# Kernel optimization log

Measured on AMD Instinct MI355X. Metric: run time of the kernel, lower is better.

Reference implementation:

```python
import jax, jax.numpy as jnp
import numpy as np

EMBED_DIM = 512
NUM_HEADS = 8
HEAD_DIM = EMBED_DIM // NUM_HEADS


def setup_inputs() -> dict:
    key = jax.random.key(0)
    k1, k2, kw, kb, kow, kob = jax.random.split(key, 6)
    B, L, C = 2, 2048, EMBED_DIM
    s = 1.0 / np.sqrt(C)
    return {
        "x1": jax.random.normal(k1, (B, L, C), dtype=jnp.float32),
        "x2": jax.random.normal(k2, (B, L, C), dtype=jnp.float32),
        # nn.Linear(embed_dim, 3*embed_dim): weight [3C, C], bias [3C]
        "qkv_w": jax.random.uniform(kw, (3 * C, C), jnp.float32, -s, s),
        "qkv_b": jax.random.uniform(kb, (3 * C,), jnp.float32, -s, s),
        # nn.Linear(embed_dim, embed_dim): weight [C, C], bias [C]
        "out_w": jax.random.uniform(kow, (C, C), jnp.float32, -s, s),
        "out_b": jax.random.uniform(kob, (C,), jnp.float32, -s, s),
    }


def _qkv(x, qkv_w, qkv_b):
    B, L, C = x.shape
    H, D = NUM_HEADS, C // NUM_HEADS
    # Linear: x @ W^T + b, then view(B, L, H, 3, D) and split along the '3' axis
    qkv = (jnp.einsum("blc,fc->blf", x, qkv_w) + qkv_b).reshape(B, L, H, 3, D)
    qkv = jnp.transpose(qkv, (3, 0, 2, 1, 4))  # [3, B, H, L, D]
    return qkv[0], qkv[1], qkv[2]


def _attend(q, k, v):
    # q,k,v: [B, H, L, D]; scale by 1/sqrt(D)
    scale = 1.0 / np.sqrt(q.shape[-1]).astype(np.float32)
    scores = jnp.einsum("bhqd,bhkd->bhqk", q, k) * scale  # [B,H,L,L]
    attn = jax.nn.softmax(scores, axis=-1)
    out = jnp.einsum("bhqk,bhkd->bhqd", attn, v)
    B, H, L, D = out.shape
    return jnp.transpose(out, (0, 2, 1, 3)).reshape(B, L, H * D)


def reference(x1, x2, qkv_w, qkv_b, out_w, out_b):
    q1, k1, v1 = _qkv(x1, qkv_w, qkv_b)
    q2, k2, v2 = _qkv(x2, qkv_w, qkv_b)
    out1 = _attend(q1, k2, v2)  # q from x1, k/v from x2
    out2 = _attend(q2, k1, v1)  # q from x2, k/v from x1
    out1 = jnp.einsum("blc,fc->blf", out1, out_w) + out_b
    out2 = jnp.einsum("blc,fc->blf", out2, out_w) + out_b
    return (out1, out2)
```

## Files before the change

### kernel.cpp

```cpp
#include <hip/hip_runtime.h>
#include <stdint.h>

typedef unsigned short u16;
typedef unsigned int u32;
typedef short bf16x8 __attribute__((ext_vector_type(8)));
typedef float f32x4 __attribute__((ext_vector_type(4)));

#define K_DIM 512

__device__ __forceinline__ u16 f2bf(float f) {
  union { float f; u32 u; } v; v.f = f;
  return (u16)((v.u + 0x8000u) >> 16);
}
__device__ __forceinline__ u32 pk2(float lo, float hi) {
  union { float f; u32 u; } a, b; a.f = lo; b.f = hi;
  return __builtin_amdgcn_perm(b.u + 0x8000u, a.u + 0x8000u, 0x07060302u);
}

__global__ void cvt_kernel(const float* __restrict__ x1, const float* __restrict__ x2,
                           const float* __restrict__ qkvw, const float* __restrict__ outw,
                           u16* __restrict__ xb, u16* __restrict__ wqkv, u16* __restrict__ wout) {
  int tid = blockIdx.x * 256 + threadIdx.x;
  const float4* src; u16* dst; int idx = tid;
  if (idx < 524288)        { src = (const float4*)x1;   dst = xb; }
  else if (idx < 1048576)  { src = (const float4*)x2;   dst = xb + 2097152; idx -= 524288; }
  else if (idx < 1245184)  { src = (const float4*)qkvw; dst = wqkv;         idx -= 1048576; }
  else                     { src = (const float4*)outw; dst = wout;         idx -= 1245184; }
  float4 v = src[idx];
  *(uint2*)&dst[idx * 4] = make_uint2(pk2(v.x, v.y), pk2(v.z, v.w));
}

#define LDA 40

__global__ __launch_bounds__(256, 3) void qkv_gemm(
    const u16* __restrict__ A, const u16* __restrict__ W, const float* __restrict__ bias,
    u16* __restrict__ qb, u16* __restrict__ kb, u16* __restrict__ vtb) {
  __shared__ __align__(16) u16 As[2][128 * LDA];
  __shared__ __align__(16) u16 Bs[2][128 * LDA];
  const int t = threadIdx.x;
  const int m0 = blockIdx.x * 128, n0 = blockIdx.y * 128;
  const int lane = t & 63, l16 = lane & 15, quad = lane >> 4;
  const int w = t >> 6;
  const int wm = (w >> 1) * 64, wn = (w & 1) * 64;
  const int sr = t >> 2, sc = (t & 3) * 8;

  const u16* Ap = A + (size_t)(m0 + sr) * K_DIM + sc;
  const u16* Wp = W + (size_t)(n0 + sr) * K_DIM + sc;

  f32x4 acc[4][4];
#pragma unroll
  for (int i = 0; i < 4; ++i)
#pragma unroll
    for (int j = 0; j < 4; ++j) acc[i][j] = (f32x4){0.f, 0.f, 0.f, 0.f};

  uint4 ra0 = *(const uint4*)(Ap);
  uint4 ra1 = *(const uint4*)(Ap + 64 * K_DIM);
  uint4 rb0 = *(const uint4*)(Wp);
  uint4 rb1 = *(const uint4*)(Wp + 64 * K_DIM);
  *(uint4*)&As[0][sr * LDA + sc] = ra0;
  *(uint4*)&As[0][(sr + 64) * LDA + sc] = ra1;
  *(uint4*)&Bs[0][sr * LDA + sc] = rb0;
  *(uint4*)&Bs[0][(sr + 64) * LDA + sc] = rb1;
  ra0 = *(const uint4*)(Ap + 32);
  ra1 = *(const uint4*)(Ap + 64 * K_DIM + 32);
  rb0 = *(const uint4*)(Wp + 32);
  rb1 = *(const uint4*)(Wp + 64 * K_DIM + 32);
  __syncthreads();

  for (int kt = 0; kt < 16; ++kt) {
    const int cur = kt & 1, nxt = cur ^ 1;
    if (kt < 15) {
      *(uint4*)&As[nxt][sr * LDA + sc] = ra0;
      *(uint4*)&As[nxt][(sr + 64) * LDA + sc] = ra1;
      *(uint4*)&Bs[nxt][sr * LDA + sc] = rb0;
      *(uint4*)&Bs[nxt][(sr + 64) * LDA + sc] = rb1;
    }
    if (kt < 14) {
      int ko = (kt + 2) * 32;
      ra0 = *(const uint4*)(Ap + ko);
      ra1 = *(const uint4*)(Ap + 64 * K_DIM + ko);
      rb0 = *(const uint4*)(Wp + ko);
      rb1 = *(const uint4*)(Wp + 64 * K_DIM + ko);
    }
    bf16x8 af[4], bfr[4];
#pragma unroll
    for (int mi = 0; mi < 4; ++mi)
      af[mi] = *(const bf16x8*)&As[cur][(wm + mi * 16 + l16) * LDA + quad * 8];
#pragma unroll
    for (int ni = 0; ni < 4; ++ni)
      bfr[ni] = *(const bf16x8*)&Bs[cur][(wn + ni * 16 + l16) * LDA + quad * 8];
#pragma unroll
    for (int mi = 0; mi < 4; ++mi)
#pragma unroll
      for (int ni = 0; ni < 4; ++ni)
        acc[mi][ni] = __builtin_amdgcn_mfma_f32_16x16x32_bf16(bfr[ni], af[mi], acc[mi][ni], 0, 0, 0);
    __syncthreads();
  }

  const int fbase = n0 + wn;
  const int h = fbase / 192;
  const int s = (fbase - h * 192) >> 6;
  float4 bv[4];
#pragma unroll
  for (int ni = 0; ni < 4; ++ni)
    bv[ni] = *(const float4*)&bias[fbase + ni * 16 + quad * 4];
  const int bh = m0 >> 11;
  const int lbase = (m0 & 2047) + wm;

  if (s == 2) {
    u16* dst = vtb + (size_t)((bh * 8 + h) * 64) * 2048;
#pragma unroll
    for (int mi = 0; mi < 4; ++mi) {
      int l = lbase + mi * 16 + l16;
#pragma unroll
      for (int ni = 0; ni < 4; ++ni)
#pragma unroll
        for (int r = 0; r < 4; ++r)
          dst[(ni * 16 + quad * 4 + r) * 2048 + l] = f2bf(acc[mi][ni][r] + bv[ni][r]);
    }
  } else {
    u16* dst = (s == 0 ? qb : kb) + (size_t)((bh * 8 + h) * 2048) * 64;
    const float sc2 = (s == 0) ? 0.18033688011112042f : 1.0f;
#pragma unroll
    for (int mi = 0; mi < 4; ++mi) {
      int l = lbase + mi * 16 + l16;
#pragma unroll
      for (int ni = 0; ni < 4; ++ni) {
        float v0 = (acc[mi][ni][0] + bv[ni][0]) * sc2;
        float v1 = (acc[mi][ni][1] + bv[ni][1]) * sc2;
        float v2 = (acc[mi][ni][2] + bv[ni][2]) * sc2;
        float v3 = (acc[mi][ni][3] + bv[ni][3]) * sc2;
        *(uint2*)&dst[(size_t)l * 64 + ni * 16 + quad * 4] = make_uint2(pk2(v0, v1), pk2(v2, v3));
      }
    }
  }
}

#define LQ 72
#define LP 72

__global__ __launch_bounds__(512, 4) void attn_kernel(
    const u16* __restrict__ qb, const u16* __restrict__ kb, const u16* __restrict__ vtb,
    u16* __restrict__ attnb) {
  __shared__ __align__(16) u16 Ks[64 * LQ];
  __shared__ __align__(16) u16 VTs[64 * LQ];
  __shared__ __align__(16) u16 Ps[128 * LP];

  const int t = threadIdx.x;
  const int w = t >> 6, lane = t & 63, l16 = lane & 15, quad = lane >> 4;
  const int bid = blockIdx.x;
  const int qt = bid & 15;
  const int comb = bid >> 4;
  const int h = comb & 7, bb = (comb >> 3) & 1, pair = comb >> 4;
  const int in_q = pair, in_kv = pair ^ 1;

  const u16* Qg = qb + (size_t)((in_q * 2 + bb) * 8 + h) * 2048 * 64;
  const u16* Kg = kb + (size_t)((in_kv * 2 + bb) * 8 + h) * 2048 * 64;
  const u16* Vg = vtb + (size_t)((in_kv * 2 + bb) * 8 + h) * 64 * 2048;

#pragma unroll
  for (int u = 0; u < 2; ++u) {
    int idx = u * 512 + t;
    int row = idx >> 3, seg = (idx & 7) * 8;
    *(uint4*)&Ps[row * LP + seg] = *(const uint4*)(Qg + (qt * 128 + row) * 64 + seg);
  }
  const int srow = t >> 3, sseg = (t & 7) * 8;
  uint4 rk = *(const uint4*)(Kg + srow * 64 + sseg);
  uint4 rv = *(const uint4*)(Vg + srow * 2048 + sseg);
  __syncthreads();

  bf16x8 qf[2];
#pragma unroll
  for (int ks = 0; ks < 2; ++ks)
    qf[ks] = *(const bf16x8*)&Ps[(w * 16 + l16) * LP + ks * 32 + quad * 8];

  f32x4 oacc[4];
  float rs = 0.f;
#pragma unroll
  for (int ni = 0; ni < 4; ++ni) oacc[ni] = (f32x4){0.f, 0.f, 0.f, 0.f};

  u16* Pw = &Ps[w * 16 * LP];

  for (int kt = 0; kt < 32; ++kt) {
    *(uint4*)&Ks[srow * LQ + sseg] = rk;
    *(uint4*)&VTs[srow * LQ + sseg] = rv;
    __syncthreads();
    if (kt < 31) {
      int ko = (kt + 1) * 64;
      rk = *(const uint4*)(Kg + (ko + srow) * 64 + sseg);
      rv = *(const uint4*)(Vg + srow * 2048 + ko + sseg);
    }

    f32x4 sacc[4];
#pragma unroll
    for (int ni = 0; ni < 4; ++ni) sacc[ni] = (f32x4){0.f, 0.f, 0.f, 0.f};
#pragma unroll
    for (int ks = 0; ks < 2; ++ks) {
      bf16x8 kfr[4];
#pragma unroll
      for (int ni = 0; ni < 4; ++ni)
        kfr[ni] = *(const bf16x8*)&Ks[(ni * 16 + l16) * LQ + ks * 32 + quad * 8];
#pragma unroll
      for (int ni = 0; ni < 4; ++ni)
        sacc[ni] = __builtin_amdgcn_mfma_f32_16x16x32_bf16(kfr[ni], qf[ks], sacc[ni], 0, 0, 0);
    }

#pragma unroll
    for (int ni = 0; ni < 4; ++ni) {
      float p0 = __builtin_amdgcn_exp2f(sacc[ni][0]);
      float p1 = __builtin_amdgcn_exp2f(sacc[ni][1]);
      float p2 = __builtin_amdgcn_exp2f(sacc[ni][2]);
      float p3 = __builtin_amdgcn_exp2f(sacc[ni][3]);
      rs += (p0 + p1) + (p2 + p3);
      *(uint2*)&Pw[l16 * LP + ni * 16 + quad * 4] = make_uint2(pk2(p0, p1), pk2(p2, p3));
    }

#pragma unroll
    for (int ks = 0; ks < 2; ++ks) {
      bf16x8 vf[4];
#pragma unroll
      for (int ni = 0; ni < 4; ++ni)
        vf[ni] = *(const bf16x8*)&VTs[(ni * 16 + l16) * LQ + ks * 32 + quad * 8];
      bf16x8 pf = *(const bf16x8*)&Pw[l16 * LP + ks * 32 + quad * 8];
#pragma unroll
      for (int ni = 0; ni < 4; ++ni)
        oacc[ni] = __builtin_amdgcn_mfma_f32_16x16x32_bf16(vf[ni], pf, oacc[ni], 0, 0, 0);
    }
    __syncthreads();
  }

  float s = rs;
  s += __shfl_xor(s, 16);
  s += __shfl_xor(s, 32);
  const float inv = 1.0f / s;
  const int row = in_q * 4096 + bb * 2048 + qt * 128 + w * 16 + l16;
#pragma unroll
  for (int ni = 0; ni < 4; ++ni) {
    float v0 = oacc[ni][0] * inv;
    float v1 = oacc[ni][1] * inv;
    float v2 = oacc[ni][2] * inv;
    float v3 = oacc[ni][3] * inv;
    *(uint2*)&attnb[(size_t)row * 512 + h * 64 + ni * 16 + quad * 4] =
        make_uint2(pk2(v0, v1), pk2(v2, v3));
  }
}

__global__ __launch_bounds__(256, 2) void out_gemm(
    const u16* __restrict__ A, const u16* __restrict__ W, const float* __restrict__ bias,
    float* __restrict__ out) {
  __shared__ __align__(16) u16 As[2][64 * LDA];
  __shared__ __align__(16) u16 Bs[2][128 * LDA];
  const int t = threadIdx.x;
  const int m0 = blockIdx.x * 64, n0 = blockIdx.y * 128;
  const int lane = t & 63, l16 = lane & 15, quad = lane >> 4;
  const int w = t >> 6;
  const int wm = (w & 1) * 32, wn = (w >> 1) * 64;
  const int ar = t >> 2, ac = (t & 3) * 8;
  const int sr = t >> 2, sc = (t & 3) * 8;

  const u16* Ap = A + (size_t)(m0 + ar) * K_DIM + ac;
  const u16* Wp = W + (size_t)(n0 + sr) * K_DIM + sc;

  f32x4 acc[2][4];
#pragma unroll
  for (int i = 0; i < 2; ++i)
#pragma unroll
    for (int j = 0; j < 4; ++j) acc[i][j] = (f32x4){0.f, 0.f, 0.f, 0.f};

  uint4 ra = *(const uint4*)Ap;
  uint4 rb0 = *(const uint4*)(Wp);
  uint4 rb1 = *(const uint4*)(Wp + 64 * K_DIM);
  *(uint4*)&As[0][ar * LDA + ac] = ra;
  *(uint4*)&Bs[0][sr * LDA + sc] = rb0;
  *(uint4*)&Bs[0][(sr + 64) * LDA + sc] = rb1;
  ra = *(const uint4*)(Ap + 32);
  rb0 = *(const uint4*)(Wp + 32);
  rb1 = *(const uint4*)(Wp + 64 * K_DIM + 32);
  __syncthreads();

  for (int kt = 0; kt < 16; ++kt) {
    const int cur = kt & 1, nxt = cur ^ 1;
    if (kt < 15) {
      *(uint4*)&As[nxt][ar * LDA + ac] = ra;
      *(uint4*)&Bs[nxt][sr * LDA + sc] = rb0;
      *(uint4*)&Bs[nxt][(sr + 64) * LDA + sc] = rb1;
    }
    if (kt < 14) {
      int ko = (kt + 2) * 32;
      ra = *(const uint4*)(Ap + ko);
      rb0 = *(const uint4*)(Wp + ko);
      rb1 = *(const uint4*)(Wp + 64 * K_DIM + ko);
    }
    bf16x8 af[2], bfr[4];
#pragma unroll
    for (int mi = 0; mi < 2; ++mi)
      af[mi] = *(const bf16x8*)&As[cur][(wm + mi * 16 + l16) * LDA + quad * 8];
#pragma unroll
    for (int ni = 0; ni < 4; ++ni)
      bfr[ni] = *(const bf16x8*)&Bs[cur][(wn + ni * 16 + l16) * LDA + quad * 8];
#pragma unroll
    for (int mi = 0; mi < 2; ++mi)
#pragma unroll
      for (int ni = 0; ni < 4; ++ni)
        acc[mi][ni] = __builtin_amdgcn_mfma_f32_16x16x32_bf16(af[mi], bfr[ni], acc[mi][ni], 0, 0, 0);
    __syncthreads();
  }

#pragma unroll
  for (int ni = 0; ni < 4; ++ni) {
    int f = n0 + wn + ni * 16 + l16;
    float bv = bias[f];
#pragma unroll
    for (int mi = 0; mi < 2; ++mi)
#pragma unroll
      for (int r = 0; r < 4; ++r) {
        int m = m0 + wm + mi * 16 + quad * 4 + r;
        out[(size_t)m * 512 + f] = acc[mi][ni][r] + bv;
      }
  }
}

extern "C" void kernel_launch(void* const* d_in, const int* in_sizes, int n_in,
                              void* d_out, int out_size, void* d_ws, size_t ws_size,
                              hipStream_t stream) {
  const float* x1   = (const float*)d_in[0];
  const float* x2   = (const float*)d_in[1];
  const float* qkvw = (const float*)d_in[2];
  const float* qkvb = (const float*)d_in[3];
  const float* outw = (const float*)d_in[4];
  const float* outb = (const float*)d_in[5];
  float* out = (float*)d_out;
  char* ws = (char*)d_ws;

  u16* xb    = (u16*)(ws + 0);
  u16* wqkv  = (u16*)(ws + 8388608);
  u16* wout  = (u16*)(ws + 9961472);
  u16* qb    = (u16*)(ws + 10485760);
  u16* kb    = (u16*)(ws + 18874368);
  u16* vtb   = (u16*)(ws + 27262976);
  u16* attnb = (u16*)(ws + 0);

  cvt_kernel<<<5120, 256, 0, stream>>>(x1, x2, qkvw, outw, xb, wqkv, wout);

  dim3 g1(64, 12);
  qkv_gemm<<<g1, 256, 0, stream>>>(xb, wqkv, qkvb, qb, kb, vtb);

  attn_kernel<<<512, 512, 0, stream>>>(qb, kb, vtb, attnb);

  dim3 g3(128, 4);
  out_gemm<<<g3, 256, 0, stream>>>(attnb, wout, outb, out);
}
```

Baseline: 164.4 us.

## Switch attention to 32x32 MFMA with 4 waves each owning 32 query rows

The attention kernel now runs 256 threads (4 waves) per block instead of 512. Each wave handles 32 query rows and uses 32x32x16 bf16 MFMA for both QK^T and PV, replacing the 16x16x32 tiles. This halves the number of LDS fragment reads of K and V per MFMA and raises the work per wave. The block index mapping also changes so that consecutive blocks cover different heads and batches rather than different query tiles. The trade-offs are fewer waves per block for hiding latency and more accumulator registers per thread.

Result: faster. 156.3 us (-4.9%).

```diff
diff --git a/kernel.cpp b/kernel.cpp
--- a/kernel.cpp
+++ b/kernel.cpp
@@ -5,6 +5,7 @@
 typedef unsigned int u32;
 typedef short bf16x8 __attribute__((ext_vector_type(8)));
 typedef float f32x4 __attribute__((ext_vector_type(4)));
+typedef float f32x16 __attribute__((ext_vector_type(16)));
 
 #define K_DIM 512
 
@@ -139,7 +140,7 @@
 #define LQ 72
 #define LP 72
 
-__global__ __launch_bounds__(512, 4) void attn_kernel(
+__global__ __launch_bounds__(256, 2) void attn_kernel(
     const u16* __restrict__ qb, const u16* __restrict__ kb, const u16* __restrict__ vtb,
     u16* __restrict__ attnb) {
   __shared__ __align__(16) u16 Ks[64 * LQ];
@@ -147,10 +148,10 @@
   __shared__ __align__(16) u16 Ps[128 * LP];
 
   const int t = threadIdx.x;
-  const int w = t >> 6, lane = t & 63, l16 = lane & 15, quad = lane >> 4;
+  const int w = t >> 6, lane = t & 63, l32 = lane & 31, h2 = lane >> 5;
   const int bid = blockIdx.x;
-  const int qt = bid & 15;
-  const int comb = bid >> 4;
+  const int comb = bid & 31;
+  const int qt = bid >> 5;
   const int h = comb & 7, bb = (comb >> 3) & 1, pair = comb >> 4;
   const int in_q = pair, in_kv = pair ^ 1;
 
@@ -159,90 +160,96 @@
   const u16* Vg = vtb + (size_t)((in_kv * 2 + bb) * 8 + h) * 64 * 2048;
 
 #pragma unroll
-  for (int u = 0; u < 2; ++u) {
-    int idx = u * 512 + t;
+  for (int u = 0; u < 4; ++u) {
+    int idx = u * 256 + t;
     int row = idx >> 3, seg = (idx & 7) * 8;
     *(uint4*)&Ps[row * LP + seg] = *(const uint4*)(Qg + (qt * 128 + row) * 64 + seg);
   }
   const int srow = t >> 3, sseg = (t & 7) * 8;
-  uint4 rk = *(const uint4*)(Kg + srow * 64 + sseg);
-  uint4 rv = *(const uint4*)(Vg + srow * 2048 + sseg);
+  uint4 rk0 = *(const uint4*)(Kg + srow * 64 + sseg);
+  uint4 rk1 = *(const uint4*)(Kg + (srow + 32) * 64 + sseg);
+  uint4 rv0 = *(const uint4*)(Vg + srow * 2048 + sseg);
+  uint4 rv1 = *(const uint4*)(Vg + (srow + 32) * 2048 + sseg);
   __syncthreads();
 
-  bf16x8 qf[2];
-#pragma unroll
-  for (int ks = 0; ks < 2; ++ks)
-    qf[ks] = *(const bf16x8*)&Ps[(w * 16 + l16) * LP + ks * 32 + quad * 8];
-
-  f32x4 oacc[4];
+  bf16x8 qf[4];
+#pragma unroll
+  for (int ks = 0; ks < 4; ++ks)
+    qf[ks] = *(const bf16x8*)&Ps[(w * 32 + l32) * LP + ks * 16 + h2 * 8];
+
+  f32x16 oacc[2];
+#pragma unroll
+  for (int mi = 0; mi < 2; ++mi)
+#pragma unroll
+    for (int r = 0; r < 16; ++r) oacc[mi][r] = 0.f;
   float rs = 0.f;
-#pragma unroll
-  for (int ni = 0; ni < 4; ++ni) oacc[ni] = (f32x4){0.f, 0.f, 0.f, 0.f};
-
-  u16* Pw = &Ps[w * 16 * LP];
+
+  u16* Pw = &Ps[w * 32 * LP];
 
   for (int kt = 0; kt < 32; ++kt) {
-    *(uint4*)&Ks[srow * LQ + sseg] = rk;
-    *(uint4*)&VTs[srow * LQ + sseg] = rv;
+    *(uint4*)&Ks[srow * LQ + sseg] = rk0;
+    *(uint4*)&Ks[(srow + 32) * LQ + sseg] = rk1;
+    *(uint4*)&VTs[srow * LQ + sseg] = rv0;
+    *(uint4*)&VTs[(srow + 32) * LQ + sseg] = rv1;
     __syncthreads();
     if (kt < 31) {
       int ko = (kt + 1) * 64;
-      rk = *(const uint4*)(Kg + (ko + srow) * 64 + sseg);
-      rv = *(const uint4*)(Vg + srow * 2048 + ko + sseg);
-    }
-
-    f32x4 sacc[4];
-#pragma unroll
-    for (int ni = 0; ni < 4; ++ni) sacc[ni] = (f32x4){0.f, 0.f, 0.f, 0.f};
-#pragma unroll
-    for (int ks = 0; ks < 2; ++ks) {
-      bf16x8 kfr[4];
-#pragma unroll
-      for (int ni = 0; ni < 4; ++ni)
-        kfr[ni] = *(const bf16x8*)&Ks[(ni * 16 + l16) * LQ + ks * 32 + quad * 8];
-#pragma unroll
-      for (int ni = 0; ni < 4; ++ni)
-        sacc[ni] = __builtin_amdgcn_mfma_f32_16x16x32_bf16(kfr[ni], qf[ks], sacc[ni], 0, 0, 0);
-    }
-
-#pragma unroll
-    for (int ni = 0; ni < 4; ++ni) {
-      float p0 = __builtin_amdgcn_exp2f(sacc[ni][0]);
-      float p1 = __builtin_amdgcn_exp2f(sacc[ni][1]);
-      float p2 = __builtin_amdgcn_exp2f(sacc[ni][2]);
-      float p3 = __builtin_amdgcn_exp2f(sacc[ni][3]);
-      rs += (p0 + p1) + (p2 + p3);
-      *(uint2*)&Pw[l16 * LP + ni * 16 + quad * 4] = make_uint2(pk2(p0, p1), pk2(p2, p3));
-    }
-
-#pragma unroll
-    for (int ks = 0; ks < 2; ++ks) {
-      bf16x8 vf[4];
-#pragma unroll
-      for (int ni = 0; ni < 4; ++ni)
-        vf[ni] = *(const bf16x8*)&VTs[(ni * 16 + l16) * LQ + ks * 32 + quad * 8];
-      bf16x8 pf = *(const bf16x8*)&Pw[l16 * LP + ks * 32 + quad * 8];
-#pragma unroll
-      for (int ni = 0; ni < 4; ++ni)
-        oacc[ni] = __builtin_amdgcn_mfma_f32_16x16x32_bf16(vf[ni], pf, oacc[ni], 0, 0, 0);
+      rk0 = *(const uint4*)(Kg + (ko + srow) * 64 + sseg);
+      rk1 = *(const uint4*)(Kg + (ko + srow + 32) * 64 + sseg);
+      rv0 = *(const uint4*)(Vg + srow * 2048 + ko + sseg);
+      rv1 = *(const uint4*)(Vg + (srow + 32) * 2048 + ko + sseg);
+    }
+
+    f32x16 sacc[2];
+#pragma unroll
+    for (int mi = 0; mi < 2; ++mi)
+#pragma unroll
+      for (int r = 0; r < 16; ++r) sacc[mi][r] = 0.f;
+#pragma unroll
+    for (int ks = 0; ks < 4; ++ks) {
+      bf16x8 kfr0 = *(const bf16x8*)&Ks[(l32) * LQ + ks * 16 + h2 * 8];
+      bf16x8 kfr1 = *(const bf16x8*)&Ks[(32 + l32) * LQ + ks * 16 + h2 * 8];
+      sacc[0] = __builtin_amdgcn_mfma_f32_32x32x16_bf16(kfr0, qf[ks], sacc[0], 0, 0, 0);
+      sacc[1] = __builtin_amdgcn_mfma_f32_32x32x16_bf16(kfr1, qf[ks], sacc[1], 0, 0, 0);
+    }
+
+#pragma unroll
+    for (int mi = 0; mi < 2; ++mi)
+#pragma unroll
+      for (int rg = 0; rg < 4; ++rg) {
+        float p0 = __builtin_amdgcn_exp2f(sacc[mi][rg * 4 + 0]);
+        float p1 = __builtin_amdgcn_exp2f(sacc[mi][rg * 4 + 1]);
+        float p2 = __builtin_amdgcn_exp2f(sacc[mi][rg * 4 + 2]);
+        float p3 = __builtin_amdgcn_exp2f(sacc[mi][rg * 4 + 3]);
+        rs += (p0 + p1) + (p2 + p3);
+        *(uint2*)&Pw[l32 * LP + mi * 32 + rg * 8 + h2 * 4] = make_uint2(pk2(p0, p1), pk2(p2, p3));
+      }
+
+#pragma unroll
+    for (int ks = 0; ks < 4; ++ks) {
+      bf16x8 pf = *(const bf16x8*)&Pw[l32 * LP + ks * 16 + h2 * 8];
+      bf16x8 vf0 = *(const bf16x8*)&VTs[(l32) * LQ + ks * 16 + h2 * 8];
+      bf16x8 vf1 = *(const bf16x8*)&VTs[(32 + l32) * LQ + ks * 16 + h2 * 8];
+      oacc[0] = __builtin_amdgcn_mfma_f32_32x32x16_bf16(vf0, pf, oacc[0], 0, 0, 0);
+      oacc[1] = __builtin_amdgcn_mfma_f32_32x32x16_bf16(vf1, pf, oacc[1], 0, 0, 0);
     }
     __syncthreads();
   }
 
-  float s = rs;
-  s += __shfl_xor(s, 16);
-  s += __shfl_xor(s, 32);
-  const float inv = 1.0f / s;
-  const int row = in_q * 4096 + bb * 2048 + qt * 128 + w * 16 + l16;
-#pragma unroll
-  for (int ni = 0; ni < 4; ++ni) {
-    float v0 = oacc[ni][0] * inv;
-    float v1 = oacc[ni][1] * inv;
-    float v2 = oacc[ni][2] * inv;
-    float v3 = oacc[ni][3] * inv;
-    *(uint2*)&attnb[(size_t)row * 512 + h * 64 + ni * 16 + quad * 4] =
-        make_uint2(pk2(v0, v1), pk2(v2, v3));
-  }
+  rs += __shfl_xor(rs, 32);
+  const float inv = 1.0f / rs;
+  const int row = in_q * 4096 + bb * 2048 + qt * 128 + w * 32 + l32;
+#pragma unroll
+  for (int mi = 0; mi < 2; ++mi)
+#pragma unroll
+    for (int rg = 0; rg < 4; ++rg) {
+      float v0 = oacc[mi][rg * 4 + 0] * inv;
+      float v1 = oacc[mi][rg * 4 + 1] * inv;
+      float v2 = oacc[mi][rg * 4 + 2] * inv;
+      float v3 = oacc[mi][rg * 4 + 3] * inv;
+      *(uint2*)&attnb[(size_t)row * 512 + h * 64 + mi * 32 + rg * 8 + h2 * 4] =
+          make_uint2(pk2(v0, v1), pk2(v2, v3));
+    }
 }
 
 __global__ __launch_bounds__(256, 2) void out_gemm(
@@ -345,7 +352,7 @@
   dim3 g1(64, 12);
   qkv_gemm<<<g1, 256, 0, stream>>>(xb, wqkv, qkvb, qb, kb, vtb);
 
-  attn_kernel<<<512, 512, 0, stream>>>(qb, kb, vtb, attnb);
+  attn_kernel<<<512, 256, 0, stream>>>(qb, kb, vtb, attnb);
 
   dim3 g3(128, 4);
   out_gemm<<<g3, 256, 0, stream>>>(attnb, wout, outb, out);
```
